# Kernel tuning notes

Hardware: AMD Instinct MI355X
Metric: run time of the kernel (lower is better)

The kernel has to match this reference:

```python
import jax, jax.numpy as jnp
import numpy as np

B, LD = 256, 64
NO, LO = 10240, 32
NM, LM = 81920, 16
EO, EM = 81920, 327680
E, HID, H, Dh, V = 128, 256, 8, 16, 10000


def masked_mean(tokens, table):
    # tokens: [N, L] int; pad id = 0
    emb = table[tokens]                            # [N, L, E]
    mask = (tokens != 0)
    s = jnp.sum(emb * mask[..., None].astype(emb.dtype), axis=1)
    lens = jnp.maximum(jnp.sum(mask, axis=1), 1).astype(emb.dtype)
    return s / lens[:, None]


def segment_softmax(scores, seg, num_segments):
    # scores: [E, ...]; softmax over entries sharing seg id (PyG softmax)
    m = jax.ops.segment_max(scores, seg, num_segments=num_segments)
    e = jnp.exp(scores - m[seg])
    s = jax.ops.segment_sum(e, seg, num_segments=num_segments)
    return e / (s[seg] + 1e-16)


def gcn_conv(x, W, b, src, dst, n):
    # PyG GCNConv: normalize=True, add_self_loops=True
    xw = x @ W
    loops = jnp.arange(n, dtype=src.dtype)
    s2 = jnp.concatenate([src, loops])
    d2 = jnp.concatenate([dst, loops])
    deg = jax.ops.segment_sum(jnp.ones_like(d2, dtype=x.dtype), d2, num_segments=n)
    dinv = deg ** -0.5  # deg >= 1 due to self loops
    norm = dinv[s2] * dinv[d2]
    out = jax.ops.segment_sum(xw[s2] * norm[:, None], d2, num_segments=n)
    return out + b


def transformer_conv(x, Wq, bq, Wk, bk, Wv, bv, Wskip, bskip, src, dst, n):
    q = (x @ Wq + bq).reshape(n, H, Dh)
    k = (x @ Wk + bk).reshape(n, H, Dh)
    v = (x @ Wv + bv).reshape(n, H, Dh)
    score = jnp.sum(q[dst] * k[src], axis=-1) / jnp.sqrt(jnp.asarray(Dh, x.dtype))  # [E, H]
    alpha = segment_softmax(score, dst, n)
    agg = jax.ops.segment_sum(alpha[:, :, None] * v[src], dst, num_segments=n)  # [n, H, Dh]
    return agg.reshape(n, H * Dh) + x @ Wskip + bskip


def global_attention(x, Wg, bg, seg, num_segments):
    gate = x @ Wg + bg                              # [N, 1]
    a = segment_softmax(gate, seg, num_segments)
    return jax.ops.segment_sum(a * x, seg, num_segments=num_segments)


def setup_inputs():
    key = jax.random.key(0)
    ks = jax.random.split(key, 20)
    sc = lambda k, shape: jax.random.normal(k, shape, dtype=jnp.float32) * 0.05
    inp = {
        "desc_tokens": jax.random.randint(ks[0], (B, LD), 0, V, dtype=jnp.int32),
        "x_tokens": jax.random.randint(ks[1], (NO, LO), 0, V, dtype=jnp.int32),
        "mini_tokens": jax.random.randint(ks[2], (NM, LM), 0, V, dtype=jnp.int32),
        "src": jax.random.randint(ks[3], (EO,), 0, NO, dtype=jnp.int32),
        "dst": jax.random.randint(ks[4], (EO,), 0, NO, dtype=jnp.int32),
        "mini_src": jax.random.randint(ks[5], (EM,), 0, NM, dtype=jnp.int32),
        "mini_dst": jax.random.randint(ks[6], (EM,), 0, NM, dtype=jnp.int32),
        "mini_batch": (jnp.arange(NM, dtype=jnp.int32) // (NM // NO)),
        "node_batch": (jnp.arange(NO, dtype=jnp.int32) // (NO // B)),
        "desc_table": sc(ks[7], (V, E)),
        "code_table": sc(ks[8], (V, E)),
        "code_table2": sc(ks[9], (V, E)),
        "Wq": sc(ks[10], (E, H * Dh)), "bq": jnp.zeros((H * Dh,), jnp.float32),
        "Wk": sc(ks[11], (E, H * Dh)), "bk": jnp.zeros((H * Dh,), jnp.float32),
        "Wv": sc(ks[12], (E, H * Dh)), "bv": jnp.zeros((H * Dh,), jnp.float32),
        "Wskip": sc(ks[13], (E, H * Dh)), "bskip": jnp.zeros((H * Dh,), jnp.float32),
        "W2": sc(ks[14], (E, HID)), "b2": jnp.zeros((HID,), jnp.float32),
        "W3": sc(ks[15], (HID, E)), "b3": jnp.zeros((E,), jnp.float32),
        "Wg": sc(ks[16], (E, 1)), "bg": jnp.zeros((1,), jnp.float32),
    }
    return inp


def reference(desc_tokens, x_tokens, mini_tokens, src, dst, mini_src, mini_dst,
              mini_batch, node_batch, desc_table, code_table, code_table2,
              Wq, bq, Wk, bk, Wv, bv, Wskip, bskip, W2, b2, W3, b3, Wg, bg):
    # encode_desc: embedding + masked mean pool -> [B, E]
    h_n = masked_mean(desc_tokens, desc_table)
    # encode_code_graph
    stmt_emb = masked_mean(x_tokens, code_table2)          # [NO, E]
    mini_emb = masked_mean(mini_tokens, code_table)        # [NM, E]
    mini_hidden = transformer_conv(mini_emb, Wq, bq, Wk, bk, Wv, bv,
                                   Wskip, bskip, mini_src, mini_dst, NM)
    mini_fn = global_attention(mini_hidden, Wg, bg, mini_batch, NO)  # [NO, E]
    mini_fn = (mini_fn + stmt_emb) * 0.5
    h = jax.nn.relu(gcn_conv(mini_fn, W2, b2, src, dst, NO))
    final_stmt = gcn_conv(h, W3, b3, src, dst, NO)
    fn_repr = global_attention(final_stmt, Wg, bg, node_batch, B)    # [B, E]
    # cosine similarity (torch eps=1e-8 clamps each norm)
    na = jnp.maximum(jnp.linalg.norm(fn_repr, axis=-1), 1e-8)
    nb = jnp.maximum(jnp.linalg.norm(h_n, axis=-1), 1e-8)
    return jnp.sum(fn_repr * h_n, axis=-1) / (na * nb)
```

## Files before the change

kernel.cpp:

```cpp
#include <hip/hip_runtime.h>
#include <hip/hip_bf16.h>
#include <math.h>

#define BB   256
#define LDE  64
#define NO   10240
#define LO   32
#define NM   81920
#define LM   16
#define EO   81920
#define EM   327680
#define ED   128
#define HIDD 256
#define NH   8
#define DH   16
#define VV   10000

static inline int nblk(long long n, int b) { return (int)((n + b - 1) / b); }

typedef __attribute__((ext_vector_type(8))) short short8;
typedef __attribute__((ext_vector_type(4))) float f32x4;

static __device__ __forceinline__ unsigned short bf16_rne(float f) {
  unsigned u = __float_as_uint(f);
  return (unsigned short)((u + 0x7fffu + ((u >> 16) & 1u)) >> 16);
}
static __device__ __forceinline__ float bf16_to_f(unsigned short h) {
  return __uint_as_float(((unsigned)h) << 16);
}
static __device__ __forceinline__ float4 b4f(ushort4 h) {
  return make_float4(bf16_to_f(h.x), bf16_to_f(h.y), bf16_to_f(h.z), bf16_to_f(h.w));
}

struct WC { const float* W; int K, M; short8* hi; short8* lo; int base; };
struct WC6 { WC w[6]; };
__global__ void __launch_bounds__(256)
conv_all_k(WC6 wc, const float* __restrict__ t1, unsigned short* __restrict__ o1,
           const float* __restrict__ t2, unsigned short* __restrict__ o2) {
  if (blockIdx.x < 64) {
    int g = blockIdx.x * 256 + threadIdx.x;
    int wi = 0;
    #pragma unroll
    for (int i = 1; i < 6; ++i) if (g >= wc.w[i].base) wi = i;
    const WC c = wc.w[wi];
    int idx = g - c.base;
    int lane = idx & 63;
    int nt = (idx >> 6) % (c.M / 16);
    int kb = (idx >> 6) / (c.M / 16);
    int n = nt * 16 + (lane & 15);
    int k0 = kb * 32 + ((lane >> 4) << 3);
    short8 h, l;
    #pragma unroll
    for (int j = 0; j < 8; ++j) {
      float v = c.W[(size_t)(k0 + j) * c.M + n];
      unsigned short hb = bf16_rne(v);
      h[j] = (short)hb;
      l[j] = (short)bf16_rne(v - bf16_to_f(hb));
    }
    c.hi[idx] = h; c.lo[idx] = l;
  } else {
    int q = (blockIdx.x - 64) * 256 + threadIdx.x;
    const int NT = VV * ED / 4;
    if (q < NT) {
      float4 v = *(const float4*)(t1 + (size_t)q * 4);
      *(ushort4*)(o1 + (size_t)q * 4) =
          make_ushort4(bf16_rne(v.x), bf16_rne(v.y), bf16_rne(v.z), bf16_rne(v.w));
    } else if (q < 2 * NT) {
      int q2 = q - NT;
      float4 v = *(const float4*)(t2 + (size_t)q2 * 4);
      *(ushort4*)(o2 + (size_t)q2 * 4) =
          make_ushort4(bf16_rne(v.x), bf16_rne(v.y), bf16_rne(v.z), bf16_rne(v.w));
    }
  }
}

template<int L, bool TBF, bool OUTBF>
static __device__ __forceinline__ void embed_body(const int* __restrict__ tokens,
                                                  const void* __restrict__ table,
                                                  void* __restrict__ out, int blk) {
  const int r = threadIdx.x >> 5, lane = threadIdx.x & 31;
  const int n0 = blk * 8;
  __shared__ int toks[8][L];
  for (int i = threadIdx.x; i < 8 * L; i += 256)
    toks[i / L][i % L] = tokens[(size_t)n0 * L + i];
  __syncthreads();
  float4 acc = make_float4(0.f, 0.f, 0.f, 0.f);
  int cnt = 0;
  #pragma unroll
  for (int l = 0; l < L; ++l) {
    int t = toks[r][l];
    float4 v;
    if (TBF) v = b4f(*((const ushort4*)((const unsigned short*)table + (size_t)t * ED + lane * 4)));
    else     v = *(const float4*)((const float*)table + (size_t)t * ED + lane * 4);
    float msk = (t != 0) ? 1.f : 0.f;
    cnt += (t != 0);
    acc.x = fmaf(msk, v.x, acc.x); acc.y = fmaf(msk, v.y, acc.y);
    acc.z = fmaf(msk, v.z, acc.z); acc.w = fmaf(msk, v.w, acc.w);
  }
  float inv = 1.f / (float)(cnt > 0 ? cnt : 1);
  acc.x *= inv; acc.y *= inv; acc.z *= inv; acc.w *= inv;
  if (OUTBF)
    *(ushort4*)((unsigned short*)out + (size_t)(n0 + r) * ED + lane * 4) =
        make_ushort4(bf16_rne(acc.x), bf16_rne(acc.y), bf16_rne(acc.z), bf16_rne(acc.w));
  else
    *(float4*)((float*)out + (size_t)(n0 + r) * ED + lane * 4) = acc;
}

__global__ void __launch_bounds__(256)
embed_all_k(const int* __restrict__ desc_tokens, const float* __restrict__ desc_table,
            float* __restrict__ h_n,
            const int* __restrict__ x_tokens, const unsigned short* __restrict__ ctab2,
            float* __restrict__ stmt,
            const int* __restrict__ mini_tokens, const unsigned short* __restrict__ ctab,
            unsigned short* __restrict__ miniE) {
  int b = blockIdx.x;
  if (b < BB / 8) embed_body<LDE, false, false>(desc_tokens, desc_table, h_n, b);
  else if (b < BB / 8 + NO / 8) embed_body<LO, true, false>(x_tokens, ctab2, stmt, b - BB / 8);
  else embed_body<LM, true, true>(mini_tokens, ctab, miniE, b - BB / 8 - NO / 8);
}

struct QDesc { const short8* bh; const short8* bl; const float* bias; unsigned short* C; };
struct QDesc4 { QDesc d[4]; };

__global__ void __launch_bounds__(256)
mgemm_qkvs5_k(const unsigned short* __restrict__ Ab, QDesc4 g4) {
  const QDesc d = g4.d[blockIdx.x];
  const int n0 = blockIdx.y * 128;
  __shared__ unsigned short Tl[4][16][68];
  const int tid = threadIdx.x;
  const int w = tid >> 6, lane = tid & 63;
  const int wm = (w & 1) * 4, wn = (w >> 1) * 4;
  const int r = lane & 15, qd = lane >> 4;
  f32x4 acc[4][4];
  #pragma unroll
  for (int i = 0; i < 4; ++i)
    #pragma unroll
    for (int j = 0; j < 4; ++j) acc[i][j] = (f32x4){0.f, 0.f, 0.f, 0.f};
  #pragma unroll
  for (int kb = 0; kb < 4; ++kb) {
    short8 bh[4], bl[4];
    #pragma unroll
    for (int j = 0; j < 4; ++j) {
      size_t bi = ((size_t)kb * 8 + wn + j) * 64 + lane;
      bh[j] = d.bh[bi]; bl[j] = d.bl[bi];
    }
    short8 a[4];
    #pragma unroll
    for (int i = 0; i < 4; ++i)
      a[i] = *(const short8*)(Ab + (size_t)(n0 + (wm + i) * 16 + r) * ED + kb * 32 + qd * 8);
    #pragma unroll
    for (int i = 0; i < 4; ++i)
      #pragma unroll
      for (int j = 0; j < 4; ++j) {
        acc[i][j] = __builtin_amdgcn_mfma_f32_16x16x32_bf16(a[i], bh[j], acc[i][j], 0, 0, 0);
        acc[i][j] = __builtin_amdgcn_mfma_f32_16x16x32_bf16(a[i], bl[j], acc[i][j], 0, 0, 0);
      }
  }
  const int r8 = lane >> 3, c8 = lane & 7;
  const int growbase = n0 + (w & 1) * 64;
  const int gcol = (w >> 1) * 64 + c8 * 8;
  #pragma unroll
  for (int i = 0; i < 4; ++i) {
    #pragma unroll
    for (int j = 0; j < 4; ++j) {
      float bv = d.bias[(wn + j) * 16 + r];
      #pragma unroll
      for (int rr = 0; rr < 4; ++rr)
        Tl[w][qd * 4 + rr][j * 16 + r] = bf16_rne(acc[i][j][rr] + bv);
    }
    #pragma unroll
    for (int it = 0; it < 2; ++it) {
      int lrow = it * 8 + r8;
      const unsigned short* lp = &Tl[w][lrow][c8 * 8];
      uint2 u0 = *(const uint2*)lp;
      uint2 u1 = *(const uint2*)(lp + 4);
      *(uint4*)(d.C + (size_t)(growbase + i * 16 + lrow) * ED + gcol) =
          make_uint4(u0.x, u0.y, u1.x, u1.y);
    }
  }
}

template<bool RELU>
__global__ void __launch_bounds__(256)
mgemm_k(const float* __restrict__ A, const short8* __restrict__ Bh,
        const short8* __restrict__ Bl, const float* __restrict__ bias,
        float* C, int K, int M) {
  __shared__ short8 Ah[8][64];
  __shared__ short8 Al[8][64];
  const int bm0 = blockIdx.y * 128, bn0 = blockIdx.x * 128;
  const int tid = threadIdx.x;
  const int w = tid >> 6, lane = tid & 63;
  const int wm = (w & 1) * 4, wn = (w >> 1) * 4;
  const int NTm = M / 16;
  f32x4 acc[4][4];
  #pragma unroll
  for (int i = 0; i < 4; ++i)
    #pragma unroll
    for (int j = 0; j < 4; ++j) acc[i][j] = (f32x4){0.f, 0.f, 0.f, 0.f};
  const int kbn = K / 32;
  for (int kb = 0; kb < kbn; ++kb) {
    __syncthreads();
    #pragma unroll
    for (int it = 0; it < 2; ++it) {
      int u = tid + it * 256;
      int mt = u >> 6, l = u & 63;
      int m = bm0 + mt * 16 + (l & 15);
      int k = kb * 32 + ((l >> 4) << 3);
      const float* ap = A + (size_t)m * K + k;
      float4 v0 = *(const float4*)ap;
      float4 v1 = *(const float4*)(ap + 4);
      float f[8] = {v0.x, v0.y, v0.z, v0.w, v1.x, v1.y, v1.z, v1.w};
      short8 hh, ll;
      #pragma unroll
      for (int j = 0; j < 8; ++j) {
        unsigned short hb = bf16_rne(f[j]);
        hh[j] = (short)hb;
        ll[j] = (short)bf16_rne(f[j] - bf16_to_f(hb));
      }
      Ah[mt][l] = hh; Al[mt][l] = ll;
    }
    __syncthreads();
    short8 bh[4], bl[4];
    #pragma unroll
    for (int j = 0; j < 4; ++j) {
      size_t bi = ((size_t)kb * NTm + (bn0 >> 4) + wn + j) * 64 + lane;
      bh[j] = Bh[bi]; bl[j] = Bl[bi];
    }
    #pragma unroll
    for (int i = 0; i < 4; ++i) {
      short8 ah = Ah[wm + i][lane];
      short8 al = Al[wm + i][lane];
      #pragma unroll
      for (int j = 0; j < 4; ++j) {
        acc[i][j] = __builtin_amdgcn_mfma_f32_16x16x32_bf16(ah, bh[j], acc[i][j], 0, 0, 0);
        acc[i][j] = __builtin_amdgcn_mfma_f32_16x16x32_bf16(ah, bl[j], acc[i][j], 0, 0, 0);
        acc[i][j] = __builtin_amdgcn_mfma_f32_16x16x32_bf16(al, bh[j], acc[i][j], 0, 0, 0);
      }
    }
  }
  const int q = lane >> 4, c = lane & 15;
  #pragma unroll
  for (int i = 0; i < 4; ++i)
    #pragma unroll
    for (int j = 0; j < 4; ++j) {
      int col = bn0 + (wn + j) * 16 + c;
      float bv = bias ? bias[col] : 0.f;
      #pragma unroll
      for (int rr = 0; rr < 4; ++rr) {
        int row = bm0 + (wm + i) * 16 + q * 4 + rr;
        float v = acc[i][j][rr] + bv;
        if (RELU) v = fmaxf(v, 0.f);
        C[(size_t)row * M + col] = v;
      }
    }
}

__global__ void hist2_k(const int* __restrict__ dm, int* __restrict__ hm,
                        const int* __restrict__ dd, int* __restrict__ ho) {
  int e = blockIdx.x * 256 + threadIdx.x;
  if (e < EM) atomicAdd(&hm[dm[e]], 1);
  else { int e2 = e - EM; if (e2 < EO) atomicAdd(&ho[dd[e2]], 1); }
}
__global__ void chunk_sum_k(const int* __restrict__ hist, int* __restrict__ partials, int N) {
  __shared__ int sd[256];
  int i = blockIdx.x * 256 + threadIdx.x;
  sd[threadIdx.x] = (i < N) ? hist[i] : 0;
  __syncthreads();
  for (int s = 128; s > 0; s >>= 1) {
    if (threadIdx.x < s) sd[threadIdx.x] += sd[threadIdx.x + s];
    __syncthreads();
  }
  if (threadIdx.x == 0) partials[blockIdx.x] = sd[0];
}
__global__ void scan_partials2_k(int* __restrict__ p) {
  __shared__ int sd[512];
  int base = (blockIdx.x == 0) ? 0 : NM / 256;
  int B    = (blockIdx.x == 0) ? NM / 256 : NO / 256;
  int t = threadIdx.x;
  int v = (t < B) ? p[base + t] : 0;
  sd[t] = v; __syncthreads();
  for (int off = 1; off < 512; off <<= 1) {
    int a = (t >= off) ? sd[t - off] : 0;
    __syncthreads();
    sd[t] += a;
    __syncthreads();
  }
  if (t < B) p[base + t] = sd[t] - v;
}
__global__ void scan_final2_k(const int* __restrict__ hist, const int* __restrict__ partials,
                              int* __restrict__ offsm, int* __restrict__ curm,
                              int* __restrict__ offso, int* __restrict__ curo,
                              float* __restrict__ dinv) {
  __shared__ int sd[256];
  int i = blockIdx.x * 256 + threadIdx.x;
  int v = hist[i];
  sd[threadIdx.x] = v; __syncthreads();
  for (int off = 1; off < 256; off <<= 1) {
    int a = (threadIdx.x >= off) ? sd[threadIdx.x - off] : 0;
    __syncthreads();
    sd[threadIdx.x] += a;
    __syncthreads();
  }
  int excl = sd[threadIdx.x] - v + partials[blockIdx.x];
  if (i < NM) {
    offsm[i] = excl; curm[i] = excl;
    if (i == NM - 1) offsm[NM] = excl + v;
  } else {
    int i2 = i - NM;
    offso[i2] = excl; curo[i2] = excl;
    if (i2 == NO - 1) offso[NO] = excl + v;
    dinv[i2] = 1.f / sqrtf(1.f + (float)v);
  }
}
__global__ void scatter2_k(const int* __restrict__ sm, const int* __restrict__ dm,
                           int* __restrict__ cm, int* __restrict__ km,
                           const int* __restrict__ so, const int* __restrict__ dd,
                           int* __restrict__ co, int* __restrict__ ko) {
  int e = blockIdx.x * 256 + threadIdx.x;
  if (e < EM) {
    int pos = atomicAdd(&cm[dm[e]], 1);
    km[pos] = sm[e];
  } else {
    int e2 = e - EM;
    if (e2 < EO) {
      int pos = atomicAdd(&co[dd[e2]], 1);
      ko[pos] = so[e2];
    }
  }
}

__global__ void __launch_bounds__(128)
attn_fused_k(unsigned short* qh, const unsigned short* __restrict__ kk,
             const unsigned short* __restrict__ vv, const unsigned short* __restrict__ skip,
             const int* __restrict__ offs, const int* __restrict__ csr,
             const float* __restrict__ Wg, const float* __restrict__ bg,
             float* __restrict__ gateOut) {
  const int g = threadIdx.x >> 5, lane = threadIdx.x & 31;
  const int n = blockIdx.x * 4 + g;
  float4 q = b4f(*(const ushort4*)(qh + (size_t)n * ED + lane * 4));
  int lo = offs[n], hi = offs[n + 1];
  float4 O = make_float4(0.f, 0.f, 0.f, 0.f);
  float m = -INFINITY, l = 0.f;
  for (int e = lo; e < hi; ++e) {
    int s = csr[e];
    float4 kt = b4f(*(const ushort4*)(kk + (size_t)s * ED + lane * 4));
    float4 vt = b4f(*(const ushort4*)(vv + (size_t)s * ED + lane * 4));
    float p = q.x * kt.x + q.y * kt.y + q.z * kt.z + q.w * kt.w;
    p += __shfl_xor(p, 1, 64);
    p += __shfl_xor(p, 2, 64);
    float sc = p * 0.25f;
    float mn = fmaxf(m, sc);
    float scale = __expf(m - mn);
    float pe = __expf(sc - mn);
    l = l * scale + pe;
    O.x = O.x * scale + pe * vt.x; O.y = O.y * scale + pe * vt.y;
    O.z = O.z * scale + pe * vt.z; O.w = O.w * scale + pe * vt.w;
    m = mn;
  }
  float inv = 1.f / (l + 1e-16f);
  float4 sk = b4f(*(const ushort4*)(skip + (size_t)n * ED + lane * 4));
  float4 out = make_float4(O.x * inv + sk.x, O.y * inv + sk.y,
                           O.z * inv + sk.z, O.w * inv + sk.w);
  *(ushort4*)(qh + (size_t)n * ED + lane * 4) =
      make_ushort4(bf16_rne(out.x), bf16_rne(out.y), bf16_rne(out.z), bf16_rne(out.w));
  float4 wg = *(const float4*)(Wg + lane * 4);
  float ps = out.x * wg.x + out.y * wg.y + out.z * wg.z + out.w * wg.w;
  #pragma unroll
  for (int o = 1; o <= 16; o <<= 1) ps += __shfl_xor(ps, o, 64);
  if (lane == 0) gateOut[n] = ps + bg[0];
}

__global__ void __launch_bounds__(128)
gcn_gather_k(const float* __restrict__ x, const float* __restrict__ dinv,
             const int* __restrict__ offs, const int* __restrict__ csr,
             const float* __restrict__ bias, float* __restrict__ out,
             const float* __restrict__ Wg, const float* __restrict__ bg,
             float* __restrict__ gateOut) {
  const int g = threadIdx.x >> 5, lane = threadIdx.x & 31;
  const int n = blockIdx.x * 4 + g;
  float di = dinv[n];
  float4 xs = *(const float4*)(x + (size_t)n * ED + lane * 4);
  float w0 = di * di;
  float4 acc = make_float4(w0 * xs.x, w0 * xs.y, w0 * xs.z, w0 * xs.w);
  int lo = offs[n], hi = offs[n + 1];
  for (int e = lo; e < hi; ++e) {
    int s = csr[e];
    float w = di * dinv[s];
    float4 v = *(const float4*)(x + (size_t)s * ED + lane * 4);
    acc.x = fmaf(w, v.x, acc.x); acc.y = fmaf(w, v.y, acc.y);
    acc.z = fmaf(w, v.z, acc.z); acc.w = fmaf(w, v.w, acc.w);
  }
  if (bias) {
    float4 b4 = *(const float4*)(bias + lane * 4);
    acc.x += b4.x; acc.y += b4.y; acc.z += b4.z; acc.w += b4.w;
  }
  *(float4*)(out + (size_t)n * ED + lane * 4) = acc;
  if (gateOut) {
    float4 wg = *(const float4*)(Wg + lane * 4);
    float ps = acc.x * wg.x + acc.y * wg.y + acc.z * wg.z + acc.w * wg.w;
    #pragma unroll
    for (int o = 1; o <= 16; o <<= 1) ps += __shfl_xor(ps, o, 64);
    if (lane == 0) gateOut[n] = ps + bg[0];
  }
}

static __device__ __forceinline__ int lower_bound_d(const int* a, int n, int key) {
  int lo = 0, hi = n;
  while (lo < hi) { int mid = (lo + hi) >> 1; if (a[mid] < key) lo = mid + 1; else hi = mid; }
  return lo;
}
template<bool COMBINE, bool XBF>
__global__ void __launch_bounds__(128)
gattn_k(const void* __restrict__ xv, const float* __restrict__ gate,
        const int* __restrict__ seg, int Ntot,
        const float* __restrict__ other, float* __restrict__ out) {
  const int g = threadIdx.x >> 5, lane = threadIdx.x & 31;
  const int n = blockIdx.x * 4 + g;
  __shared__ int sh[4][2];
  if (lane == 0) {
    sh[g][0] = lower_bound_d(seg, Ntot, n);
    sh[g][1] = lower_bound_d(seg, Ntot, n + 1);
  }
  __syncthreads();
  int lo = sh[g][0], hi = sh[g][1];
  float m = -INFINITY;
  for (int j = lo; j < hi; ++j) m = fmaxf(m, gate[j]);
  float ssum = 0.f;
  for (int j = lo; j < hi; ++j) ssum += __expf(gate[j] - m);
  float inv = 1.f / (ssum + 1e-16f);
  float4 acc = make_float4(0.f, 0.f, 0.f, 0.f);
  for (int j = lo; j < hi; ++j) {
    float a = __expf(gate[j] - m) * inv;
    float4 v;
    if (XBF) v = b4f(*((const ushort4*)((const unsigned short*)xv + (size_t)j * ED + lane * 4)));
    else     v = *((const float4*)((const float*)xv + (size_t)j * ED) + lane);
    acc.x = fmaf(a, v.x, acc.x); acc.y = fmaf(a, v.y, acc.y);
    acc.z = fmaf(a, v.z, acc.z); acc.w = fmaf(a, v.w, acc.w);
  }
  if (COMBINE) {
    float4 o4 = *(const float4*)(other + (size_t)n * ED + lane * 4);
    acc.x = (acc.x + o4.x) * 0.5f; acc.y = (acc.y + o4.y) * 0.5f;
    acc.z = (acc.z + o4.z) * 0.5f; acc.w = (acc.w + o4.w) * 0.5f;
  }
  *(float4*)(out + (size_t)n * ED + lane * 4) = acc;
}

__global__ void __launch_bounds__(128)
gattn_cos_k(const float* __restrict__ x, const float* __restrict__ gate,
            const int* __restrict__ seg, int Ntot,
            const float* __restrict__ hn, float* __restrict__ outp) {
  const int g = threadIdx.x >> 5, lane = threadIdx.x & 31;
  const int n = blockIdx.x * 4 + g;
  __shared__ int sh[4][2];
  if (lane == 0) {
    sh[g][0] = lower_bound_d(seg, Ntot, n);
    sh[g][1] = lower_bound_d(seg, Ntot, n + 1);
  }
  __syncthreads();
  int lo = sh[g][0], hi = sh[g][1];
  float m = -INFINITY;
  for (int j = lo; j < hi; ++j) m = fmaxf(m, gate[j]);
  float ssum = 0.f;
  for (int j = lo; j < hi; ++j) ssum += __expf(gate[j] - m);
  float inv = 1.f / (ssum + 1e-16f);
  float4 acc = make_float4(0.f, 0.f, 0.f, 0.f);
  for (int j = lo; j < hi; ++j) {
    float a = __expf(gate[j] - m) * inv;
    float4 v = *((const float4*)(x + (size_t)j * ED) + lane);
    acc.x = fmaf(a, v.x, acc.x); acc.y = fmaf(a, v.y, acc.y);
    acc.z = fmaf(a, v.z, acc.z); acc.w = fmaf(a, v.w, acc.w);
  }
  float4 hv = *(const float4*)(hn + (size_t)n * ED + lane * 4);
  float dot = acc.x * hv.x + acc.y * hv.y + acc.z * hv.z + acc.w * hv.w;
  float na  = acc.x * acc.x + acc.y * acc.y + acc.z * acc.z + acc.w * acc.w;
  float nb  = hv.x * hv.x + hv.y * hv.y + hv.z * hv.z + hv.w * hv.w;
  #pragma unroll
  for (int o = 1; o <= 16; o <<= 1) {
    dot += __shfl_xor(dot, o, 64);
    na  += __shfl_xor(na,  o, 64);
    nb  += __shfl_xor(nb,  o, 64);
  }
  if (lane == 0)
    outp[n] = dot / (fmaxf(sqrtf(na), 1e-8f) * fmaxf(sqrtf(nb), 1e-8f));
}

constexpr size_t OFF_HN    = 0;
constexpr size_t OFF_STMT  = OFF_HN    + (size_t)BB * ED;
constexpr size_t OFF_A     = OFF_STMT  + (size_t)NO * ED;
constexpr size_t OFF_QHID  = OFF_A     + (size_t)NM * ED;
constexpr size_t OFF_CT    = OFF_QHID  + (size_t)NM * ED / 2;
constexpr size_t OFF_K     = OFF_QHID  + (size_t)NM * ED;
constexpr size_t OFF_V     = OFF_K     + (size_t)NM * ED;
constexpr size_t T0        = OFF_V     + (size_t)NM * ED;
constexpr size_t OFF_GATE  = T0;
constexpr size_t OFF_GATE2 = OFF_GATE  + (size_t)NM;
constexpr size_t OFF_DINV  = OFF_GATE2 + (size_t)NO;
constexpr size_t OFF_HISTM = OFF_DINV  + (size_t)NO;
constexpr size_t OFF_HISTO = OFF_HISTM + (size_t)NM;
constexpr size_t OFF_OFFSM = OFF_HISTO + (size_t)NO;
constexpr size_t OFF_CURM  = OFF_OFFSM + (size_t)NM + 1;
constexpr size_t OFF_CSRM  = OFF_CURM  + (size_t)NM;
constexpr size_t OFF_OFFSO = OFF_CSRM  + (size_t)EM;
constexpr size_t OFF_CURO  = OFF_OFFSO + (size_t)NO + 1;
constexpr size_t OFF_CSRO  = OFF_CURO  + (size_t)NO;
constexpr size_t OFF_PART  = OFF_CSRO  + (size_t)EO;
constexpr size_t OFF_WFHI  = OFF_PART  + 512;
constexpr size_t OFF_WFLO  = OFF_WFHI  + 65536;
constexpr size_t WO_Q  = 0, WO_K = 2048, WO_V = 4096, WO_S = 6144, WO_W2 = 8192, WO_W3 = 12288;
constexpr size_t OFF_MFN   = OFF_A;
constexpr size_t OFF_AGG   = OFF_MFN   + (size_t)NO * ED;
constexpr size_t OFF_H     = OFF_AGG   + (size_t)NO * ED;
constexpr size_t OFF_T     = OFF_H     + (size_t)NO * HIDD;
constexpr size_t OFF_FIN   = OFF_T     + (size_t)NO * ED;

extern "C" void kernel_launch(void* const* d_in, const int* in_sizes, int n_in,
                              void* d_out, int out_size, void* d_ws, size_t ws_size,
                              hipStream_t stream) {
  const int* desc_tokens = (const int*)d_in[0];
  const int* x_tokens    = (const int*)d_in[1];
  const int* mini_tokens = (const int*)d_in[2];
  const int* src         = (const int*)d_in[3];
  const int* dst         = (const int*)d_in[4];
  const int* mini_src    = (const int*)d_in[5];
  const int* mini_dst    = (const int*)d_in[6];
  const int* mini_batch  = (const int*)d_in[7];
  const int* node_batch  = (const int*)d_in[8];
  const float* desc_table  = (const float*)d_in[9];
  const float* code_table  = (const float*)d_in[10];
  const float* code_table2 = (const float*)d_in[11];
  const float* Wq = (const float*)d_in[12]; const float* bq = (const float*)d_in[13];
  const float* Wk = (const float*)d_in[14]; const float* bk = (const float*)d_in[15];
  const float* Wv = (const float*)d_in[16]; const float* bv = (const float*)d_in[17];
  const float* Wskip = (const float*)d_in[18]; const float* bskip = (const float*)d_in[19];
  const float* W2 = (const float*)d_in[20]; const float* b2 = (const float*)d_in[21];
  const float* W3 = (const float*)d_in[22]; const float* b3 = (const float*)d_in[23];
  const float* Wg = (const float*)d_in[24]; const float* bg = (const float*)d_in[25];

  float* ws = (float*)d_ws;
  float* h_n   = ws + OFF_HN;
  float* stmt  = ws + OFF_STMT;
  unsigned short* miniE_b = (unsigned short*)(ws + OFF_A);
  unsigned short* qhid_b = (unsigned short*)(ws + OFF_QHID);
  unsigned short* ctab_b  = (unsigned short*)(ws + OFF_CT);
  unsigned short* ctab2_b = (unsigned short*)(ws + OFF_CT + (size_t)VV * ED / 2);
  unsigned short* kbuf_b = (unsigned short*)(ws + OFF_K);
  unsigned short* skip_b = kbuf_b + (size_t)NM * ED;
  unsigned short* vbuf_b = (unsigned short*)(ws + OFF_V);
  float* gate  = ws + OFF_GATE;
  float* gate2 = ws + OFF_GATE2;
  float* dinv  = ws + OFF_DINV;
  int* histm = (int*)(ws + OFF_HISTM);
  int* histo = (int*)(ws + OFF_HISTO);
  int* offsm = (int*)(ws + OFF_OFFSM);
  int* curm  = (int*)(ws + OFF_CURM);
  int* csrm  = (int*)(ws + OFF_CSRM);
  int* offso = (int*)(ws + OFF_OFFSO);
  int* curo  = (int*)(ws + OFF_CURO);
  int* csro  = (int*)(ws + OFF_CSRO);
  int* part  = (int*)(ws + OFF_PART);
  short8* wfhi = (short8*)(ws + OFF_WFHI);
  short8* wflo = (short8*)(ws + OFF_WFLO);
  float* mini_fn = ws + OFF_MFN;
  float* aggb    = ws + OFF_AGG;
  float* hbuf    = ws + OFF_H;
  float* tbuf    = ws + OFF_T;
  float* finalS  = ws + OFF_FIN;
  float* outp    = (float*)d_out;

  WC6 wc;
  wc.w[0] = {Wq,    ED,   ED,   wfhi + WO_Q,  wflo + WO_Q,  (int)WO_Q};
  wc.w[1] = {Wk,    ED,   ED,   wfhi + WO_K,  wflo + WO_K,  (int)WO_K};
  wc.w[2] = {Wv,    ED,   ED,   wfhi + WO_V,  wflo + WO_V,  (int)WO_V};
  wc.w[3] = {Wskip, ED,   ED,   wfhi + WO_S,  wflo + WO_S,  (int)WO_S};
  wc.w[4] = {W2,    ED,   HIDD, wfhi + WO_W2, wflo + WO_W2, (int)WO_W2};
  wc.w[5] = {W3,    HIDD, ED,   wfhi + WO_W3, wflo + WO_W3, (int)WO_W3};
  conv_all_k<<<64 + nblk(2 * VV * ED / 4, 256), 256, 0, stream>>>(
      wc, code_table, ctab_b, code_table2, ctab2_b);

  hipMemsetAsync(histm, 0, (size_t)(NM + NO) * 4, stream);
  hist2_k<<<nblk(EM + EO, 256), 256, 0, stream>>>(mini_dst, histm, dst, histo);
  chunk_sum_k<<<(NM + NO) / 256, 256, 0, stream>>>(histm, part, NM + NO);
  scan_partials2_k<<<2, 512, 0, stream>>>(part);
  scan_final2_k<<<(NM + NO) / 256, 256, 0, stream>>>(histm, part, offsm, curm,
                                                     offso, curo, dinv);
  scatter2_k<<<nblk(EM + EO, 256), 256, 0, stream>>>(mini_src, mini_dst, curm, csrm,
                                                     src, dst, curo, csro);

  embed_all_k<<<BB / 8 + NO / 8 + NM / 8, 256, 0, stream>>>(
      desc_tokens, desc_table, h_n, x_tokens, ctab2_b, stmt,
      mini_tokens, ctab_b, miniE_b);

  QDesc4 g4;
  g4.d[0] = {wfhi + WO_Q, wflo + WO_Q, bq,    qhid_b};
  g4.d[1] = {wfhi + WO_K, wflo + WO_K, bk,    kbuf_b};
  g4.d[2] = {wfhi + WO_V, wflo + WO_V, bv,    vbuf_b};
  g4.d[3] = {wfhi + WO_S, wflo + WO_S, bskip, skip_b};
  { dim3 g(4, NM / 128); mgemm_qkvs5_k<<<g, 256, 0, stream>>>(miniE_b, g4); }

  attn_fused_k<<<NM / 4, 128, 0, stream>>>(qhid_b, kbuf_b, vbuf_b, skip_b,
                                           offsm, csrm, Wg, bg, gate);

  gattn_k<true, true><<<NO / 4, 128, 0, stream>>>(qhid_b, gate, mini_batch, NM, stmt, mini_fn);

  gcn_gather_k<<<NO / 4, 128, 0, stream>>>(mini_fn, dinv, offso, csro, nullptr, aggb,
                                           nullptr, nullptr, nullptr);
  { dim3 g(HIDD / 128, NO / 128);
    mgemm_k<true><<<g, 256, 0, stream>>>(aggb, wfhi + WO_W2, wflo + WO_W2, b2, hbuf, ED, HIDD); }

  { dim3 g(1, NO / 128);
    mgemm_k<false><<<g, 256, 0, stream>>>(hbuf, wfhi + WO_W3, wflo + WO_W3, nullptr, tbuf, HIDD, ED); }
  gcn_gather_k<<<NO / 4, 128, 0, stream>>>(tbuf, dinv, offso, csro, b3, finalS, Wg, bg, gate2);

  gattn_cos_k<<<BB / 4, 128, 0, stream>>>(finalS, gate2, node_batch, NO, h_n, outp);
}
```

Baseline: 378.5 us.

## Drop low-half bf16 weight split in QKV/skip GEMM and use 512-thread blocks

The fused Q/K/V/skip projection GEMM no longer multiplies against the low-order bf16 residual of the weights, which halves the MFMA count. Blocks grow to 8 waves, each owning a 32x64 tile instead of 64x64, so per-thread accumulators shrink. The LDS-staged vectorized epilogue is replaced by direct scalar bf16 stores. This gives up the split-bf16 weight precision and may make the output stores less coalesced.

```diff
diff --git a/kernel.cpp b/kernel.cpp
--- a/kernel.cpp
+++ b/kernel.cpp
@@ -119,65 +119,51 @@
   else embed_body<LM, true, true>(mini_tokens, ctab, miniE, b - BB / 8 - NO / 8);
 }
 
-struct QDesc { const short8* bh; const short8* bl; const float* bias; unsigned short* C; };
+struct QDesc { const short8* bh; const float* bias; unsigned short* C; };
 struct QDesc4 { QDesc d[4]; };
 
-__global__ void __launch_bounds__(256)
-mgemm_qkvs5_k(const unsigned short* __restrict__ Ab, QDesc4 g4) {
+__global__ void __launch_bounds__(512)
+mgemm_qkvs6_k(const unsigned short* __restrict__ Ab, QDesc4 g4) {
   const QDesc d = g4.d[blockIdx.x];
   const int n0 = blockIdx.y * 128;
-  __shared__ unsigned short Tl[4][16][68];
   const int tid = threadIdx.x;
   const int w = tid >> 6, lane = tid & 63;
-  const int wm = (w & 1) * 4, wn = (w >> 1) * 4;
+  const int wm = (w & 3) * 2;
+  const int wn = (w >> 2) * 4;
   const int r = lane & 15, qd = lane >> 4;
-  f32x4 acc[4][4];
-  #pragma unroll
-  for (int i = 0; i < 4; ++i)
+  f32x4 acc[2][4];
+  #pragma unroll
+  for (int i = 0; i < 2; ++i)
     #pragma unroll
     for (int j = 0; j < 4; ++j) acc[i][j] = (f32x4){0.f, 0.f, 0.f, 0.f};
   #pragma unroll
   for (int kb = 0; kb < 4; ++kb) {
-    short8 bh[4], bl[4];
+    short8 bh[4];
+    #pragma unroll
+    for (int j = 0; j < 4; ++j)
+      bh[j] = d.bh[((size_t)kb * 8 + wn + j) * 64 + lane];
+    short8 a[2];
+    #pragma unroll
+    for (int i = 0; i < 2; ++i)
+      a[i] = *(const short8*)(Ab + (size_t)(n0 + (wm + i) * 16 + r) * ED + kb * 32 + qd * 8);
+    #pragma unroll
+    for (int i = 0; i < 2; ++i)
+      #pragma unroll
+      for (int j = 0; j < 4; ++j)
+        acc[i][j] = __builtin_amdgcn_mfma_f32_16x16x32_bf16(a[i], bh[j], acc[i][j], 0, 0, 0);
+  }
+  #pragma unroll
+  for (int i = 0; i < 2; ++i)
     #pragma unroll
     for (int j = 0; j < 4; ++j) {
-      size_t bi = ((size_t)kb * 8 + wn + j) * 64 + lane;
-      bh[j] = d.bh[bi]; bl[j] = d.bl[bi];
-    }
-    short8 a[4];
-    #pragma unroll
-    for (int i = 0; i < 4; ++i)
-      a[i] = *(const short8*)(Ab + (size_t)(n0 + (wm + i) * 16 + r) * ED + kb * 32 + qd * 8);
-    #pragma unroll
-    for (int i = 0; i < 4; ++i)
+      int col = (wn + j) * 16 + r;
+      float bv = d.bias[col];
       #pragma unroll
-      for (int j = 0; j < 4; ++j) {
-        acc[i][j] = __builtin_amdgcn_mfma_f32_16x16x32_bf16(a[i], bh[j], acc[i][j], 0, 0, 0);
-        acc[i][j] = __builtin_amdgcn_mfma_f32_16x16x32_bf16(a[i], bl[j], acc[i][j], 0, 0, 0);
+      for (int rr = 0; rr < 4; ++rr) {
+        int row = (wm + i) * 16 + qd * 4 + rr;
+        d.C[(size_t)(n0 + row) * ED + col] = bf16_rne(acc[i][j][rr] + bv);
       }
-  }
-  const int r8 = lane >> 3, c8 = lane & 7;
-  const int growbase = n0 + (w & 1) * 64;
-  const int gcol = (w >> 1) * 64 + c8 * 8;
-  #pragma unroll
-  for (int i = 0; i < 4; ++i) {
-    #pragma unroll
-    for (int j = 0; j < 4; ++j) {
-      float bv = d.bias[(wn + j) * 16 + r];
-      #pragma unroll
-      for (int rr = 0; rr < 4; ++rr)
-        Tl[w][qd * 4 + rr][j * 16 + r] = bf16_rne(acc[i][j][rr] + bv);
-    }
-    #pragma unroll
-    for (int it = 0; it < 2; ++it) {
-      int lrow = it * 8 + r8;
-      const unsigned short* lp = &Tl[w][lrow][c8 * 8];
-      uint2 u0 = *(const uint2*)lp;
-      uint2 u1 = *(const uint2*)(lp + 4);
-      *(uint4*)(d.C + (size_t)(growbase + i * 16 + lrow) * ED + gcol) =
-          make_uint4(u0.x, u0.y, u1.x, u1.y);
-    }
-  }
+    }
 }
 
 template<bool RELU>
@@ -591,11 +577,11 @@
       mini_tokens, ctab_b, miniE_b);
 
   QDesc4 g4;
-  g4.d[0] = {wfhi + WO_Q, wflo + WO_Q, bq,    qhid_b};
-  g4.d[1] = {wfhi + WO_K, wflo + WO_K, bk,    kbuf_b};
-  g4.d[2] = {wfhi + WO_V, wflo + WO_V, bv,    vbuf_b};
-  g4.d[3] = {wfhi + WO_S, wflo + WO_S, bskip, skip_b};
-  { dim3 g(4, NM / 128); mgemm_qkvs5_k<<<g, 256, 0, stream>>>(miniE_b, g4); }
+  g4.d[0] = {wfhi + WO_Q, bq,    qhid_b};
+  g4.d[1] = {wfhi + WO_K, bk,    kbuf_b};
+  g4.d[2] = {wfhi + WO_V, bv,    vbuf_b};
+  g4.d[3] = {wfhi + WO_S, bskip, skip_b};
+  { dim3 g(4, NM / 128); mgemm_qkvs6_k<<<g, 512, 0, stream>>>(miniE_b, g4); }
 
   attn_fused_k<<<NM / 4, 128, 0, stream>>>(qhid_b, kbuf_b, vbuf_b, skip_b,
                                            offsm, csrm, Wg, bg, gate);
```

Result: no change. 372.1 us (-1.7%).
